# Kernel optimization log

Measured on AMD Instinct MI355X. Metric: run time of the kernel, lower is better.

The kernel has to match this reference:

```python
import jax, jax.numpy as jnp
import numpy as np

IN_FEATURES = 4096
OUT_FEATURES = 4096
N_TOKENS = 1024

@jax.custom_vjp
def binarize(w):
    # UnipolarSte.forward: (w > 0).float()
    return (w > 0).astype(w.dtype)

def _bin_fwd(w):
    return binarize(w), None

def _bin_bwd(_, g):
    # UnipolarSte.backward: F.hardtanh(grad_output) == clip(g, -1, 1)
    return (jnp.clip(g, -1.0, 1.0),)

binarize.defvjp(_bin_fwd, _bin_bwd)

def setup_inputs() -> dict:
    key = jax.random.key(0)
    kx, kw = jax.random.split(key)
    x = jax.random.normal(kx, (N_TOKENS, IN_FEATURES), dtype=jnp.float32)
    weight = jax.random.normal(kw, (OUT_FEATURES, IN_FEATURES), dtype=jnp.float32)
    scaling_factor = jnp.ones((OUT_FEATURES,), dtype=jnp.float32)
    return {"x": x, "weight": weight, "scaling_factor": scaling_factor}

def reference(x, weight, scaling_factor):
    w_b = binarize(weight)                      # [out, in] in {0,1}
    out = jnp.einsum('ni,oi->no', x, w_b)       # F.linear(x, w_b)
    # s_eff = round(clamp(s,1)).detach() - s.detach() + s
    s_round = jax.lax.stop_gradient(jnp.round(jnp.clip(scaling_factor, 1.0, None)))
    s_eff = s_round - jax.lax.stop_gradient(scaling_factor) + scaling_factor
    return out * s_eff[None, :]
```

## Files before the change

kernel.cpp:

```cpp
#include <hip/hip_runtime.h>

#define M_TOK 1024
#define NOUT  4096
#define KIN   4096

typedef __attribute__((ext_vector_type(8))) short bf16x8_t;
typedef __attribute__((ext_vector_type(4))) float f32x4_t;


__global__ __launch_bounds__(256) void prep_w(const float* __restrict__ w,
                                              unsigned long long* __restrict__ wbits) {
  const int lane = threadIdx.x & 63;
  const int row  = blockIdx.x * 4 + (threadIdx.x >> 6);
  const float* wr = w + (size_t)row * KIN;
  unsigned long long mine = 0;
#pragma unroll 16
  for (int q = 0; q < 64; ++q) {
    float v = wr[q * 64 + lane];
    unsigned long long m = __ballot(v > 0.f);
    if (lane == q) mine = m;
  }
  wbits[(size_t)row * 64 + lane] = mine;
}

__global__ __launch_bounds__(256) void prep_w2(const unsigned long long* __restrict__ wbits,
                                               unsigned short* __restrict__ bfrag) {
  const unsigned t = blockIdx.x * 256 + threadIdx.x;
  const int l = t & 63, kt = (t >> 6) & 63, n16 = t >> 12;
  const int row = n16 * 16 + (l & 15), quad = l >> 4;
  unsigned long long w64 = wbits[(size_t)row * 64 + kt];
  unsigned b0 = (unsigned)(w64 >> (quad * 8)) & 0xFFu;
  unsigned b1 = (unsigned)(w64 >> (quad * 8 + 32)) & 0xFFu;
  bfrag[t] = (unsigned short)(b0 | (b1 << 8));
}

__device__ __forceinline__ unsigned pack_bf16(float a, float b) {
  unsigned ua = __float_as_uint(a);
  unsigned ub = __float_as_uint(b);
  ua = (ua + 0x7FFFu + ((ua >> 16) & 1u)) >> 16;
  ub = (ub + 0x7FFFu + ((ub >> 16) & 1u)) >> 16;
  return ua | (ub << 16);
}

__global__ __launch_bounds__(256) void prep_x(const float4* __restrict__ x4,
                                              uint4* __restrict__ xfrag) {
  const unsigned t = blockIdx.x * 256 + threadIdx.x;
  const int l = t & 63;
  const unsigned f = t >> 6;
  const int m16 = f >> 7, k32 = f & 127;
  const int row = m16 * 16 + (l & 15);
  const int c4  = k32 * 8 + (l >> 4) * 2;
  const float4* p = x4 + (size_t)row * (KIN / 4) + c4;
  float4 a = p[0], b = p[1];
  uint4 o;
  o.x = pack_bf16(a.x, a.y);
  o.y = pack_bf16(a.z, a.w);
  o.z = pack_bf16(b.x, b.y);
  o.w = pack_bf16(b.z, b.w);
  xfrag[t] = o;
}

__global__ __launch_bounds__(256, 2) void gemm_bin_kernel(
    const unsigned short* __restrict__ Xf,
    const unsigned short* __restrict__ Bf,
    const float* __restrict__ sf,
    float* __restrict__ C) {
  const int tid  = threadIdx.x;
  const int lane = tid & 63;
  const int wave = tid >> 6;
  const int quad = lane >> 4;
  const int l16  = lane & 15;
  const unsigned bid = blockIdx.x;
  const int xcd = bid & 7, idx = bid >> 3;
  const int m0 = (xcd * 2 + (idx >> 5)) * 64;
  const int n0 = (idx & 31) * 128;
  const int wn = wave * 32;
  const int m16b = m0 >> 4;
  const int n16b = (n0 + wn) >> 4;

  const uint4* Xf4 = (const uint4*)Xf;

  f32x4_t acc[4][2];
#pragma unroll
  for (int i = 0; i < 4; ++i)
#pragma unroll
    for (int j = 0; j < 2; ++j)
      acc[i][j] = (f32x4_t){0.f, 0.f, 0.f, 0.f};

  auto load_kt = [&](uint4 (&ar)[4][2], unsigned (&br)[2], int kt) {
#pragma unroll
    for (int i = 0; i < 4; ++i)
#pragma unroll
      for (int ks = 0; ks < 2; ++ks)
        ar[i][ks] = Xf4[((size_t)(m16b + i) * 128 + kt * 2 + ks) * 64 + lane];
#pragma unroll
    for (int j = 0; j < 2; ++j)
      br[j] = Bf[((n16b + j) * 64 + kt) * 64 + lane];
  };

  auto compute = [&](uint4 (&ar)[4][2], unsigned (&br)[2]) {
#pragma unroll
    for (int j = 0; j < 2; ++j)
#pragma unroll
      for (int ks = 0; ks < 2; ++ks) {
        unsigned byte = (br[j] >> (ks * 8)) & 0xFFu;
        union { unsigned u[4]; bf16x8_t v; } ex;
#pragma unroll
        for (int p = 0; p < 4; ++p) {
          unsigned tt = (byte >> (2 * p)) & 3u;
          ex.u[p] = ((tt | (tt << 15)) & 0x10001u) * 0x3F80u;
        }
#pragma unroll
        for (int i = 0; i < 4; ++i) {
          union { uint4 q; bf16x8_t v; } av;
          av.q = ar[i][ks];
          acc[i][j] = __builtin_amdgcn_mfma_f32_16x16x32_bf16(av.v, ex.v, acc[i][j], 0, 0, 0);
        }
      }
  };

  uint4 aA[4][2], aB[4][2];
  unsigned bA[2], bB[2];
  load_kt(aA, bA, 0);
  for (int kt = 0; kt < 64; kt += 2) {
    load_kt(aB, bB, kt + 1);
    compute(aA, bA);
    if (kt + 2 < 64) load_kt(aA, bA, kt + 2);
    compute(aB, bB);
  }

#pragma unroll
  for (int j = 0; j < 2; ++j) {
    const int n = n0 + wn + j * 16 + l16;
    const float s = rintf(fmaxf(sf[n], 1.0f));
#pragma unroll
    for (int i = 0; i < 4; ++i) {
      const int mr = m0 + i * 16 + quad * 4;
#pragma unroll
      for (int r = 0; r < 4; ++r)
        C[(size_t)(mr + r) * NOUT + n] = acc[i][j][r] * s;
    }
  }
}

extern "C" void kernel_launch(void* const* d_in, const int* in_sizes, int n_in,
                              void* d_out, int out_size, void* d_ws, size_t ws_size,
                              hipStream_t stream) {
  const float* x  = (const float*)d_in[0];
  const float* w  = (const float*)d_in[1];
  const float* sf = (const float*)d_in[2];
  float* out = (float*)d_out;

  unsigned short*     Bfrag = (unsigned short*)d_ws;
  unsigned long long* Wbits = (unsigned long long*)((char*)d_ws + (2u << 20));
  unsigned short*     Xfrag = (unsigned short*)((char*)d_ws + (4u << 20));

  prep_w<<<1024, 256, 0, stream>>>(w, Wbits);
  prep_w2<<<4096, 256, 0, stream>>>(Wbits, Bfrag);
  prep_x<<<2048, 256, 0, stream>>>((const float4*)x, (uint4*)Xfrag);

  gemm_bin_kernel<<<512, 256, 0, stream>>>(Xfrag, Bfrag, sf, out);
}
```

Measured before the change: 153.3 us.

## Merge weight and activation prep kernels and retile GEMM to 128x64 blocks

Combines the weight-binarize and activation bf16-packing prep kernels into a single launch, saving one kernel launch and letting the two independent passes overlap. The GEMM is retiled so each block covers 128 rows by 64 columns, with each wave owning 16 output columns across 8 row tiles. This reuses each B fragment across 8 MFMAs instead of 4, but every wave now loads all eight A tiles itself. The bit-to-bf16 expansion now produces 2.0 (0x4000) with fewer ALU ops, and the epilogue scale is halved to compensate. The new tiling raises per-wave A traffic and register pressure, and the pipeline now double-buffers only half a k-step.

```diff
diff --git a/kernel.cpp b/kernel.cpp
--- a/kernel.cpp
+++ b/kernel.cpp
@@ -8,19 +8,46 @@
 typedef __attribute__((ext_vector_type(4))) float f32x4_t;
 
 
-__global__ __launch_bounds__(256) void prep_w(const float* __restrict__ w,
-                                              unsigned long long* __restrict__ wbits) {
-  const int lane = threadIdx.x & 63;
-  const int row  = blockIdx.x * 4 + (threadIdx.x >> 6);
-  const float* wr = w + (size_t)row * KIN;
-  unsigned long long mine = 0;
+__device__ __forceinline__ unsigned pack_bf16(float a, float b) {
+  unsigned ua = __float_as_uint(a);
+  unsigned ub = __float_as_uint(b);
+  ua = (ua + 0x7FFFu + ((ua >> 16) & 1u)) >> 16;
+  ub = (ub + 0x7FFFu + ((ub >> 16) & 1u)) >> 16;
+  return ua | (ub << 16);
+}
+
+__global__ __launch_bounds__(256) void prep_wx(const float* __restrict__ w,
+                                               unsigned long long* __restrict__ wbits,
+                                               const float4* __restrict__ x4,
+                                               uint4* __restrict__ xfrag) {
+  if (blockIdx.x < 1024) {
+    const int lane = threadIdx.x & 63;
+    const int row  = blockIdx.x * 4 + (threadIdx.x >> 6);
+    const float* wr = w + (size_t)row * KIN;
+    unsigned long long mine = 0;
 #pragma unroll 16
-  for (int q = 0; q < 64; ++q) {
-    float v = wr[q * 64 + lane];
-    unsigned long long m = __ballot(v > 0.f);
-    if (lane == q) mine = m;
+    for (int q = 0; q < 64; ++q) {
+      float v = wr[q * 64 + lane];
+      unsigned long long m = __ballot(v > 0.f);
+      if (lane == q) mine = m;
+    }
+    wbits[(size_t)row * 64 + lane] = mine;
+  } else {
+    const unsigned t = (blockIdx.x - 1024) * 256 + threadIdx.x;
+    const int l = t & 63;
+    const unsigned f = t >> 6;
+    const int m16 = f >> 7, k32 = f & 127;
+    const int row = m16 * 16 + (l & 15);
+    const int c4  = k32 * 8 + (l >> 4) * 2;
+    const float4* p = x4 + (size_t)row * (KIN / 4) + c4;
+    float4 a = p[0], b = p[1];
+    uint4 o;
+    o.x = pack_bf16(a.x, a.y);
+    o.y = pack_bf16(a.z, a.w);
+    o.z = pack_bf16(b.x, b.y);
+    o.w = pack_bf16(b.z, b.w);
+    xfrag[t] = o;
   }
-  wbits[(size_t)row * 64 + lane] = mine;
 }
 
 __global__ __launch_bounds__(256) void prep_w2(const unsigned long long* __restrict__ wbits,
@@ -32,32 +59,6 @@
   unsigned b0 = (unsigned)(w64 >> (quad * 8)) & 0xFFu;
   unsigned b1 = (unsigned)(w64 >> (quad * 8 + 32)) & 0xFFu;
   bfrag[t] = (unsigned short)(b0 | (b1 << 8));
-}
-
-__device__ __forceinline__ unsigned pack_bf16(float a, float b) {
-  unsigned ua = __float_as_uint(a);
-  unsigned ub = __float_as_uint(b);
-  ua = (ua + 0x7FFFu + ((ua >> 16) & 1u)) >> 16;
-  ub = (ub + 0x7FFFu + ((ub >> 16) & 1u)) >> 16;
-  return ua | (ub << 16);
-}
-
-__global__ __launch_bounds__(256) void prep_x(const float4* __restrict__ x4,
-                                              uint4* __restrict__ xfrag) {
-  const unsigned t = blockIdx.x * 256 + threadIdx.x;
-  const int l = t & 63;
-  const unsigned f = t >> 6;
-  const int m16 = f >> 7, k32 = f & 127;
-  const int row = m16 * 16 + (l & 15);
-  const int c4  = k32 * 8 + (l >> 4) * 2;
-  const float4* p = x4 + (size_t)row * (KIN / 4) + c4;
-  float4 a = p[0], b = p[1];
-  uint4 o;
-  o.x = pack_bf16(a.x, a.y);
-  o.y = pack_bf16(a.z, a.w);
-  o.z = pack_bf16(b.x, b.y);
-  o.w = pack_bf16(b.z, b.w);
-  xfrag[t] = o;
 }
 
 __global__ __launch_bounds__(256, 2) void gemm_bin_kernel(
@@ -72,74 +73,59 @@
   const int l16  = lane & 15;
   const unsigned bid = blockIdx.x;
   const int xcd = bid & 7, idx = bid >> 3;
-  const int m0 = (xcd * 2 + (idx >> 5)) * 64;
-  const int n0 = (idx & 31) * 128;
-  const int wn = wave * 32;
+  const int m0  = xcd * 128;
+  const int n0  = idx * 64;
   const int m16b = m0 >> 4;
-  const int n16b = (n0 + wn) >> 4;
+  const int n16  = (n0 >> 4) + wave;
 
   const uint4* Xf4 = (const uint4*)Xf;
 
-  f32x4_t acc[4][2];
+  f32x4_t acc[8];
 #pragma unroll
-  for (int i = 0; i < 4; ++i)
+  for (int i = 0; i < 8; ++i) acc[i] = (f32x4_t){0.f, 0.f, 0.f, 0.f};
+
+  auto loadA = [&](uint4 (&a)[8], int h) {
 #pragma unroll
-    for (int j = 0; j < 2; ++j)
-      acc[i][j] = (f32x4_t){0.f, 0.f, 0.f, 0.f};
-
-  auto load_kt = [&](uint4 (&ar)[4][2], unsigned (&br)[2], int kt) {
+    for (int i = 0; i < 8; ++i)
+      a[i] = Xf4[((m16b + i) * 128 + h) * 64 + lane];
+  };
+  auto loadB = [&](int kt) -> unsigned {
+    return (unsigned)Bf[(n16 * 64 + kt) * 64 + lane];
+  };
+  auto computeHalf = [&](uint4 (&a)[8], unsigned br, int ks) {
+    union { unsigned u[4]; bf16x8_t v; } ex;
 #pragma unroll
-    for (int i = 0; i < 4; ++i)
+    for (int p = 0; p < 4; ++p)
+      ex.u[p] = ((br << (14 - 8 * ks - 2 * p)) | (br << (29 - 8 * ks - 2 * p))) & 0x40004000u;
 #pragma unroll
-      for (int ks = 0; ks < 2; ++ks)
-        ar[i][ks] = Xf4[((size_t)(m16b + i) * 128 + kt * 2 + ks) * 64 + lane];
-#pragma unroll
-    for (int j = 0; j < 2; ++j)
-      br[j] = Bf[((n16b + j) * 64 + kt) * 64 + lane];
+    for (int i = 0; i < 8; ++i) {
+      union { uint4 q; bf16x8_t v; } av;
+      av.q = a[i];
+      acc[i] = __builtin_amdgcn_mfma_f32_16x16x32_bf16(av.v, ex.v, acc[i], 0, 0, 0);
+    }
   };
 
-  auto compute = [&](uint4 (&ar)[4][2], unsigned (&br)[2]) {
-#pragma unroll
-    for (int j = 0; j < 2; ++j)
-#pragma unroll
-      for (int ks = 0; ks < 2; ++ks) {
-        unsigned byte = (br[j] >> (ks * 8)) & 0xFFu;
-        union { unsigned u[4]; bf16x8_t v; } ex;
-#pragma unroll
-        for (int p = 0; p < 4; ++p) {
-          unsigned tt = (byte >> (2 * p)) & 3u;
-          ex.u[p] = ((tt | (tt << 15)) & 0x10001u) * 0x3F80u;
-        }
-#pragma unroll
-        for (int i = 0; i < 4; ++i) {
-          union { uint4 q; bf16x8_t v; } av;
-          av.q = ar[i][ks];
-          acc[i][j] = __builtin_amdgcn_mfma_f32_16x16x32_bf16(av.v, ex.v, acc[i][j], 0, 0, 0);
-        }
-      }
-  };
-
-  uint4 aA[4][2], aB[4][2];
-  unsigned bA[2], bB[2];
-  load_kt(aA, bA, 0);
-  for (int kt = 0; kt < 64; kt += 2) {
-    load_kt(aB, bB, kt + 1);
-    compute(aA, bA);
-    if (kt + 2 < 64) load_kt(aA, bA, kt + 2);
-    compute(aB, bB);
+  uint4 a0[8], a1[8];
+  unsigned b0, b1 = 0;
+  loadA(a0, 0);
+  b0 = loadB(0);
+  for (int kt = 0; kt < 64; ++kt) {
+    loadA(a1, 2 * kt + 1);
+    if (kt + 1 < 64) b1 = loadB(kt + 1);
+    computeHalf(a0, b0, 0);
+    if (kt + 1 < 64) loadA(a0, 2 * kt + 2);
+    computeHalf(a1, b0, 1);
+    b0 = b1;
   }
 
+  const int n = n0 + wave * 16 + l16;
+  const float s = rintf(fmaxf(sf[n], 1.0f)) * 0.5f;
 #pragma unroll
-  for (int j = 0; j < 2; ++j) {
-    const int n = n0 + wn + j * 16 + l16;
-    const float s = rintf(fmaxf(sf[n], 1.0f));
+  for (int i = 0; i < 8; ++i) {
+    const int mr = m0 + i * 16 + quad * 4;
 #pragma unroll
-    for (int i = 0; i < 4; ++i) {
-      const int mr = m0 + i * 16 + quad * 4;
-#pragma unroll
-      for (int r = 0; r < 4; ++r)
-        C[(size_t)(mr + r) * NOUT + n] = acc[i][j][r] * s;
-    }
+    for (int r = 0; r < 4; ++r)
+      C[(size_t)(mr + r) * NOUT + n] = acc[i][r] * s;
   }
 }
 
@@ -155,9 +141,7 @@
   unsigned long long* Wbits = (unsigned long long*)((char*)d_ws + (2u << 20));
   unsigned short*     Xfrag = (unsigned short*)((char*)d_ws + (4u << 20));
 
-  prep_w<<<1024, 256, 0, stream>>>(w, Wbits);
+  prep_wx<<<3072, 256, 0, stream>>>(w, Wbits, (const float4*)x, (uint4*)Xfrag);
   prep_w2<<<4096, 256, 0, stream>>>(Wbits, Bfrag);
-  prep_x<<<2048, 256, 0, stream>>>((const float4*)x, (uint4*)Xfrag);
-
   gemm_bin_kernel<<<512, 256, 0, stream>>>(Xfrag, Bfrag, sf, out);
 }
```

Result: slower. 175.7 us (+14.6%).

## Fuse weight and activation prep into one kernel and deepen GEMM prefetch

Applied to the files above, without the earlier changes.

Three prep kernels become one. Weight sign bits are now transposed into the MFMA fragment layout in shared memory, so the intermediate global bit array and one launch are no longer needed. The GEMM main loop now keeps four k-tile register buffers instead of two, giving more loads in flight. The bit-to-bf16 expansion now uses fewer ALU ops: it emits 2.0 instead of 1.0 and halves the scale in the epilogue to compensate. The deeper prefetch raises register pressure, which could lower occupancy or cause spills.

```diff
diff --git a/kernel.cpp b/kernel.cpp
--- a/kernel.cpp
+++ b/kernel.cpp
@@ -8,32 +8,6 @@
 typedef __attribute__((ext_vector_type(4))) float f32x4_t;
 
 
-__global__ __launch_bounds__(256) void prep_w(const float* __restrict__ w,
-                                              unsigned long long* __restrict__ wbits) {
-  const int lane = threadIdx.x & 63;
-  const int row  = blockIdx.x * 4 + (threadIdx.x >> 6);
-  const float* wr = w + (size_t)row * KIN;
-  unsigned long long mine = 0;
-#pragma unroll 16
-  for (int q = 0; q < 64; ++q) {
-    float v = wr[q * 64 + lane];
-    unsigned long long m = __ballot(v > 0.f);
-    if (lane == q) mine = m;
-  }
-  wbits[(size_t)row * 64 + lane] = mine;
-}
-
-__global__ __launch_bounds__(256) void prep_w2(const unsigned long long* __restrict__ wbits,
-                                               unsigned short* __restrict__ bfrag) {
-  const unsigned t = blockIdx.x * 256 + threadIdx.x;
-  const int l = t & 63, kt = (t >> 6) & 63, n16 = t >> 12;
-  const int row = n16 * 16 + (l & 15), quad = l >> 4;
-  unsigned long long w64 = wbits[(size_t)row * 64 + kt];
-  unsigned b0 = (unsigned)(w64 >> (quad * 8)) & 0xFFu;
-  unsigned b1 = (unsigned)(w64 >> (quad * 8 + 32)) & 0xFFu;
-  bfrag[t] = (unsigned short)(b0 | (b1 << 8));
-}
-
 __device__ __forceinline__ unsigned pack_bf16(float a, float b) {
   unsigned ua = __float_as_uint(a);
   unsigned ub = __float_as_uint(b);
@@ -42,22 +16,56 @@
   return ua | (ub << 16);
 }
 
-__global__ __launch_bounds__(256) void prep_x(const float4* __restrict__ x4,
-                                              uint4* __restrict__ xfrag) {
-  const unsigned t = blockIdx.x * 256 + threadIdx.x;
-  const int l = t & 63;
-  const unsigned f = t >> 6;
-  const int m16 = f >> 7, k32 = f & 127;
-  const int row = m16 * 16 + (l & 15);
-  const int c4  = k32 * 8 + (l >> 4) * 2;
-  const float4* p = x4 + (size_t)row * (KIN / 4) + c4;
-  float4 a = p[0], b = p[1];
-  uint4 o;
-  o.x = pack_bf16(a.x, a.y);
-  o.y = pack_bf16(a.z, a.w);
-  o.z = pack_bf16(b.x, b.y);
-  o.w = pack_bf16(b.z, b.w);
-  xfrag[t] = o;
+__global__ __launch_bounds__(256) void prep_wx(const float* __restrict__ w,
+                                               unsigned short* __restrict__ bfrag,
+                                               const float4* __restrict__ x4,
+                                               uint4* __restrict__ xfrag) {
+  __shared__ unsigned long long lbits[16][65];
+  const int tid  = threadIdx.x;
+  const int lane = tid & 63;
+  const int wave = tid >> 6;
+
+  if (blockIdx.x < 256) {
+    const int n16 = blockIdx.x;
+#pragma unroll 1
+    for (int rr = 0; rr < 16; ++rr) {
+      const float* wr = w + (size_t)(n16 * 16 + rr) * KIN + wave * 1024;
+      unsigned long long mine = 0;
+#pragma unroll 16
+      for (int q = 0; q < 16; ++q) {
+        float v = wr[q * 64 + lane];
+        unsigned long long m = __ballot(v > 0.f);
+        if (lane == q) mine = m;
+      }
+      if (lane < 16) lbits[rr][wave * 16 + lane] = mine;
+    }
+    __syncthreads();
+#pragma unroll
+    for (int it = 0; it < 16; ++it) {
+      const int idx = it * 256 + tid;
+      const int l = idx & 63, kt = idx >> 6;
+      const unsigned long long w64 = lbits[l & 15][kt];
+      const int quad = l >> 4;
+      const unsigned b0 = (unsigned)(w64 >> (quad * 8)) & 0xFFu;
+      const unsigned b1 = (unsigned)(w64 >> (quad * 8 + 32)) & 0xFFu;
+      bfrag[(size_t)n16 * 4096 + idx] = (unsigned short)(b0 | (b1 << 8));
+    }
+  } else {
+    const unsigned t = (blockIdx.x - 256) * 256 + tid;
+    const int l = t & 63;
+    const unsigned f = t >> 6;
+    const int m16 = f >> 7, k32 = f & 127;
+    const int row = m16 * 16 + (l & 15);
+    const int c4  = k32 * 8 + (l >> 4) * 2;
+    const float4* p = x4 + (size_t)row * (KIN / 4) + c4;
+    float4 a = p[0], b = p[1];
+    uint4 o;
+    o.x = pack_bf16(a.x, a.y);
+    o.y = pack_bf16(a.z, a.w);
+    o.z = pack_bf16(b.x, b.y);
+    o.w = pack_bf16(b.z, b.w);
+    xfrag[t] = o;
+  }
 }
 
 __global__ __launch_bounds__(256, 2) void gemm_bin_kernel(
@@ -87,52 +95,57 @@
     for (int j = 0; j < 2; ++j)
       acc[i][j] = (f32x4_t){0.f, 0.f, 0.f, 0.f};
 
-  auto load_kt = [&](uint4 (&ar)[4][2], unsigned (&br)[2], int kt) {
+  uint4 a[4][4][2];
+  unsigned b[4][2];
+
+  auto LOAD = [&](int u, int kt) {
 #pragma unroll
     for (int i = 0; i < 4; ++i)
 #pragma unroll
       for (int ks = 0; ks < 2; ++ks)
-        ar[i][ks] = Xf4[((size_t)(m16b + i) * 128 + kt * 2 + ks) * 64 + lane];
+        a[u][i][ks] = Xf4[((size_t)(m16b + i) * 128 + kt * 2 + ks) * 64 + lane];
 #pragma unroll
     for (int j = 0; j < 2; ++j)
-      br[j] = Bf[((n16b + j) * 64 + kt) * 64 + lane];
+      b[u][j] = (unsigned)Bf[((n16b + j) * 64 + kt) * 64 + lane];
   };
 
-  auto compute = [&](uint4 (&ar)[4][2], unsigned (&br)[2]) {
+  auto COMP = [&](int u) {
 #pragma unroll
     for (int j = 0; j < 2; ++j)
 #pragma unroll
       for (int ks = 0; ks < 2; ++ks) {
-        unsigned byte = (br[j] >> (ks * 8)) & 0xFFu;
-        union { unsigned u[4]; bf16x8_t v; } ex;
+        const unsigned br = b[u][j];
+        union { unsigned u32[4]; bf16x8_t v; } ex;
 #pragma unroll
-        for (int p = 0; p < 4; ++p) {
-          unsigned tt = (byte >> (2 * p)) & 3u;
-          ex.u[p] = ((tt | (tt << 15)) & 0x10001u) * 0x3F80u;
-        }
+        for (int p = 0; p < 4; ++p)
+          ex.u32[p] = ((br << (14 - 8 * ks - 2 * p)) |
+                       (br << (29 - 8 * ks - 2 * p))) & 0x40004000u;
 #pragma unroll
         for (int i = 0; i < 4; ++i) {
           union { uint4 q; bf16x8_t v; } av;
-          av.q = ar[i][ks];
+          av.q = a[u][i][ks];
           acc[i][j] = __builtin_amdgcn_mfma_f32_16x16x32_bf16(av.v, ex.v, acc[i][j], 0, 0, 0);
         }
       }
   };
 
-  uint4 aA[4][2], aB[4][2];
-  unsigned bA[2], bB[2];
-  load_kt(aA, bA, 0);
-  for (int kt = 0; kt < 64; kt += 2) {
-    load_kt(aB, bB, kt + 1);
-    compute(aA, bA);
-    if (kt + 2 < 64) load_kt(aA, bA, kt + 2);
-    compute(aB, bB);
+  LOAD(0, 0);
+  LOAD(1, 1);
+  for (int kt = 0; kt < 64; kt += 4) {
+    LOAD(2, kt + 2);
+    COMP(0);
+    LOAD(3, kt + 3);
+    COMP(1);
+    if (kt + 4 < 64) LOAD(0, kt + 4);
+    COMP(2);
+    if (kt + 5 < 64) LOAD(1, kt + 5);
+    COMP(3);
   }
 
 #pragma unroll
   for (int j = 0; j < 2; ++j) {
     const int n = n0 + wn + j * 16 + l16;
-    const float s = rintf(fmaxf(sf[n], 1.0f));
+    const float s = rintf(fmaxf(sf[n], 1.0f)) * 0.5f;
 #pragma unroll
     for (int i = 0; i < 4; ++i) {
       const int mr = m0 + i * 16 + quad * 4;
@@ -151,13 +164,9 @@
   const float* sf = (const float*)d_in[2];
   float* out = (float*)d_out;
 
-  unsigned short*     Bfrag = (unsigned short*)d_ws;
-  unsigned long long* Wbits = (unsigned long long*)((char*)d_ws + (2u << 20));
-  unsigned short*     Xfrag = (unsigned short*)((char*)d_ws + (4u << 20));
+  unsigned short* Bfrag = (unsigned short*)d_ws;
+  unsigned short* Xfrag = (unsigned short*)((char*)d_ws + (4u << 20));
 
-  prep_w<<<1024, 256, 0, stream>>>(w, Wbits);
-  prep_w2<<<4096, 256, 0, stream>>>(Wbits, Bfrag);
-  prep_x<<<2048, 256, 0, stream>>>((const float4*)x, (uint4*)Xfrag);
-
+  prep_wx<<<2304, 256, 0, stream>>>(w, Bfrag, (const float4*)x, (uint4*)Xfrag);
   gemm_bin_kernel<<<512, 256, 0, stream>>>(Xfrag, Bfrag, sf, out);
 }
```

After: 159.1 us. 3.8% more time.
